# Performance work log

Hardware: AMD Instinct MI355X
Metric: run time of the kernel (lower is better)

Reference implementation:

```python
import jax, jax.numpy as jnp
from jax import lax
import numpy as np

K = 3  # kernel size per dim, dimension=6 -> 3**6 = 729 taps
OFFS = np.stack(np.meshgrid(*([np.arange(K)] * 6), indexing='ij'), axis=-1).reshape(-1, 6).astype(np.int32)


def conv6d(x, kernel):
    """Dense emulation of a 1->1 channel MinkowskiConvolution over 6 spatial dims.

    x: (b, s, s, d, d, d, d) with zeros at absent sparse coordinates.
    kernel: (729,) flattened 3^6 kernel (in=out=1 channel, no bias).
    Zeros at absent coordinates contribute nothing to the gathered sums, so the
    dense conv equals the sparse conv evaluated everywhere.
    """
    xp = jnp.pad(x, [(0, 0)] + [(1, 1)] * 6)
    offs = jnp.asarray(OFFS)
    zero = jnp.int32(0)

    def body(acc, ow):
        off, wt = ow
        sl = lax.dynamic_slice(
            xp, (zero, off[0], off[1], off[2], off[3], off[4], off[5]), x.shape)
        return acc + wt * sl, None

    acc, _ = lax.scan(jax.checkpoint(body), jnp.zeros_like(x), (offs, kernel))
    return acc


def _transpose6d(t):
    # swap the two scale dims and the two image-coordinate pairs:
    # (b, s1, s2, h1, w1, h2, w2) -> (b, s2, s1, h2, w2, h1, w1)
    return jnp.transpose(t, (0, 2, 1, 5, 6, 3, 4))


def setup_inputs() -> dict:
    key = jax.random.key(0)
    k1, k2 = jax.random.split(key)
    x = jax.random.normal(k1, (1, 2, 2, 32, 32, 32, 32), dtype=jnp.float32)
    kernel = jax.random.normal(k2, (K ** 6,), dtype=jnp.float32) * 0.05
    return {"x": x, "kernel": kernel}


def reference(x, kernel):
    # MinkowskiConvolution outputs at the input coordinate set; MinkowskiSigmoid
    # acts on features at those coordinates; to_dense() zero-fills elsewhere.
    # Dense equivalent: mask to the input nonzero set.
    mask = (x != 0).astype(x.dtype)
    branch = lambda z: jax.nn.sigmoid(conv6d(jax.nn.relu(z), kernel))
    # symmetric mode: conv(x) + T(conv(T(x))); T(coords(T(x))) == coords(x)
    y = mask * (branch(x) + _transpose6d(branch(_transpose6d(x))))
    b, s1, s2, d1, d2, d3, d4 = y.shape
    y = y.reshape(b, s1 * s2, d1, d2, d3, d4).sum(axis=1)  # (b, h1, w1, h2, w2)
    return y
```

## Files before the change

### kernel.cpp

```cpp
#include <hip/hip_runtime.h>

typedef _Float16 h2 __attribute__((ext_vector_type(2)));

#define X_SLAB   1048576
#define PAD_S3   34
#define PAD_S2   (34*34)
#define PAD_S1   (34*34*34)
#define PAD_SLAB (34*34*34*34)
#define TAB2_ELEMS (2*81*8)
#define TAB_ELEMS  (4*81*8)

__global__ __launch_bounds__(256)
void prep(const float* __restrict__ x, const float* __restrict__ w,
          h2* __restrict__ rp2, h2* __restrict__ tab2) {
    unsigned gid = blockIdx.x * 256 + threadIdx.x;
    const unsigned total = 2u * PAD_SLAB;
    if (gid < total) {
        unsigned q = gid;
        int j4 = q % 34; q /= 34;
        int j3 = q % 34; q /= 34;
        int j2 = q % 34; q /= 34;
        int j1 = q % 34; q /= 34;
        int tp = q;
        float a = 0.f, b = 0.f;
        if (j1 >= 1 && j1 <= 32 && j2 >= 1 && j2 <= 32 &&
            j3 >= 1 && j3 <= 32 && j4 >= 1 && j4 <= 32) {
            size_t off = (size_t)(j1-1)*32768 + (j2-1)*1024 + (j3-1)*32 + (j4-1);
            a = fmaxf(x[(size_t)(2*tp  )*X_SLAB + off], 0.f);
            b = fmaxf(x[(size_t)(2*tp+1)*X_SLAB + off], 0.f);
        }
        h2 hv; hv.x = (_Float16)a; hv.y = (_Float16)b;
        rp2[gid] = hv;
    }
    if (blockIdx.x == 0) {
        for (int idx = threadIdx.x; idx < TAB2_ELEMS; idx += 256) {
            int n  = idx & 7;
            int r  = idx >> 3;
            int p5 = r % 3; r /= 3;
            int p4 = r % 3; r /= 3;
            int p3 = r % 3; r /= 3;
            int p2 = r % 3; r /= 3;
            int tp = r;
            int br = n & 1, s = n >> 1, s1 = s >> 1, s2 = s & 1;
            float vv[2];
            #pragma unroll
            for (int dt = 0; dt < 2; ++dt) {
                int t = 2*tp + dt, t1 = t >> 1, t2 = t & 1;
                int a2 = t1 - s1 + 1, b2 = t2 - s2 + 1;
                int widx = (br == 0)
                    ? (a2*243 + b2*81 + p2*27 + p3*9 + p4*3 + p5)
                    : (b2*243 + a2*81 + p4*27 + p5*9 + p2*3 + p3);
                vv[dt] = w[widx];
            }
            h2 hw; hw.x = (_Float16)vv[0]; hw.y = (_Float16)vv[1];
            tab2[idx] = hw;
        }
    }
}

__global__ __launch_bounds__(256)
void conv_dot2(const float* __restrict__ x,
               const h2* __restrict__ rp2,
               const h2* __restrict__ tab2,
               float* __restrict__ out) {
    const int e4 = threadIdx.x;
    const int e3 = blockIdx.x * 8 + threadIdx.y;
    const int e2 = blockIdx.y;
    const int e1 = blockIdx.z;

    float acc[8];
    #pragma unroll
    for (int n = 0; n < 8; ++n) acc[n] = 0.f;

    #pragma unroll 1
    for (int tp = 0; tp < 2; ++tp) {
        const h2* st  = rp2 + (size_t)tp * PAD_SLAB;
        const h2* wt0 = tab2 + tp * 648;
        #pragma unroll
        for (int p2 = 0; p2 < 3; ++p2) {
            #pragma unroll
            for (int p3 = 0; p3 < 3; ++p3) {
                const h2* base = st + ((e1+p2)*PAD_S1 + (e2+p3)*PAD_S2
                                       + e3*PAD_S3 + e4);
                const h2* wt = wt0 + (p2*3 + p3) * 72;
                #pragma unroll
                for (int p4 = 0; p4 < 3; ++p4) {
                    #pragma unroll
                    for (int p5 = 0; p5 < 3; ++p5) {
                        h2 v = base[p4*PAD_S3 + p5];
                        const h2* w8 = wt + (p4*3 + p5)*8;
                        #pragma unroll
                        for (int n = 0; n < 8; ++n)
                            acc[n] = __builtin_amdgcn_fdot2(v, w8[n], acc[n], false);
                    }
                }
            }
        }
    }

    const size_t eflat = (size_t)e1*32768 + e2*1024 + e3*32 + e4;
    float res = 0.f;
    #pragma unroll
    for (int i = 0; i < 4; ++i) {
        float xv = x[(size_t)i * X_SLAB + eflat];
        float s0 = __builtin_amdgcn_rcpf(1.f + __expf(-acc[2*i]));
        float s1 = __builtin_amdgcn_rcpf(1.f + __expf(-acc[2*i+1]));
        float m  = (xv != 0.f) ? 1.f : 0.f;
        res = fmaf(m, s0 + s1, res);
    }
    out[eflat] = res;
}

__global__ void build_wtab(const float* __restrict__ w, float* __restrict__ tab) {
    int idx = blockIdx.x * blockDim.x + threadIdx.x;
    if (idx >= TAB_ELEMS) return;
    int n  = idx & 7;
    int r  = idx >> 3;
    int p5 = r % 3; r /= 3;
    int p4 = r % 3; r /= 3;
    int p3 = r % 3; r /= 3;
    int p2 = r % 3; r /= 3;
    int t  = r;
    int t1 = t >> 1, t2 = t & 1;
    int br = n & 1;
    int s  = n >> 1;
    int s1 = s >> 1, s2 = s & 1;
    int a = t1 - s1 + 1;
    int b = t2 - s2 + 1;
    int widx = (br == 0)
        ? (a*243 + b*81 + p2*27 + p3*9 + p4*3 + p5)
        : (b*243 + a*81 + p4*27 + p5*9 + p2*3 + p3);
    tab[idx] = w[widx];
}

__global__ __launch_bounds__(256)
void conv_fp32(const float* __restrict__ x,
               const float* __restrict__ tab,
               float* __restrict__ out) {
    const int e4 = threadIdx.x;
    const int e3 = blockIdx.x * 8 + threadIdx.y;
    const int e2 = blockIdx.y;
    const int e1 = blockIdx.z;

    float acc[8];
    #pragma unroll
    for (int n = 0; n < 8; ++n) acc[n] = 0.f;

    #pragma unroll 1
    for (int t = 0; t < 4; ++t) {
        const float* st  = x + (size_t)t * X_SLAB;
        const float* wt0 = tab + t * 648;
        #pragma unroll
        for (int p2 = 0; p2 < 3; ++p2) {
            #pragma unroll
            for (int p3 = 0; p3 < 3; ++p3) {
                int i1 = e1 + p2 - 1, i2 = e2 + p3 - 1;
                bool v12 = ((unsigned)i1 < 32u) && ((unsigned)i2 < 32u);
                const float* base = st + (i1*32768 + i2*1024 + (e3-1)*32 + (e4-1));
                const float* wt = wt0 + (p2*3 + p3) * 72;
                #pragma unroll
                for (int p4 = 0; p4 < 3; ++p4) {
                    int i3 = e3 + p4 - 1;
                    bool v3 = v12 && ((unsigned)i3 < 32u);
                    #pragma unroll
                    for (int p5 = 0; p5 < 3; ++p5) {
                        int i4 = e4 + p5 - 1;
                        bool ok = v3 && ((unsigned)i4 < 32u);
                        float v = ok ? fmaxf(base[p4*32 + p5], 0.f) : 0.f;
                        const float* w8 = wt + (p4*3 + p5)*8;
                        #pragma unroll
                        for (int n = 0; n < 8; ++n)
                            acc[n] = fmaf(w8[n], v, acc[n]);
                    }
                }
            }
        }
    }

    const size_t eflat = (size_t)e1*32768 + e2*1024 + e3*32 + e4;
    float res = 0.f;
    #pragma unroll
    for (int i = 0; i < 4; ++i) {
        float xv = x[(size_t)i * X_SLAB + eflat];
        float s0 = __builtin_amdgcn_rcpf(1.f + __expf(-acc[2*i]));
        float s1 = __builtin_amdgcn_rcpf(1.f + __expf(-acc[2*i+1]));
        float m  = (xv != 0.f) ? 1.f : 0.f;
        res = fmaf(m, s0 + s1, res);
    }
    out[eflat] = res;
}

extern "C" void kernel_launch(void* const* d_in, const int* in_sizes, int n_in,
                              void* d_out, int out_size, void* d_ws, size_t ws_size,
                              hipStream_t stream) {
    const float* x = (const float*)d_in[0];
    const float* w = (const float*)d_in[1];
    float* out = (float*)d_out;

    const size_t need = 16384 + (size_t)2 * PAD_SLAB * sizeof(h2);
    dim3 blk(32, 8, 1), grd(4, 32, 32);

    if (ws_size >= need) {
        h2* tab2 = (h2*)d_ws;
        h2* rp2  = (h2*)((char*)d_ws + 16384);
        unsigned total = 2u * PAD_SLAB;
        prep<<<dim3((total + 255)/256), dim3(256), 0, stream>>>(x, w, rp2, tab2);
        conv_dot2<<<grd, blk, 0, stream>>>(x, rp2, tab2, out);
    } else {
        float* tab = (float*)d_ws;
        build_wtab<<<dim3((TAB_ELEMS + 255)/256), dim3(256), 0, stream>>>(w, tab);
        conv_fp32<<<grd, blk, 0, stream>>>(x, tab, out);
    }
}
```

Baseline: 114.5 us.

## Register-block four outputs per thread in fp16 dot2 conv with vector row loads

Each thread of the packed-fp16 convolution now computes four consecutive outputs along the innermost dimension. For each kernel row it loads three 8-byte vectors of padded input and reuses them across the three innermost taps, which removes redundant per-tap global loads. The launch shape changes to a 2D grid of 1024 blocks, and the mask load and output store are widened to float4. The cost is more accumulator registers per thread (32 floats) and a quarter as many threads, so occupancy and latency hiding may drop.

```diff
diff --git a/kernel.cpp b/kernel.cpp
--- a/kernel.cpp
+++ b/kernel.cpp
@@ -1,6 +1,8 @@
 #include <hip/hip_runtime.h>
 
 typedef _Float16 h2 __attribute__((ext_vector_type(2)));
+typedef _Float16 h4 __attribute__((ext_vector_type(4)));
+typedef float f4 __attribute__((ext_vector_type(4)));
 
 #define X_SLAB   1048576
 #define PAD_S3   34
@@ -63,52 +65,71 @@
                const h2* __restrict__ rp2,
                const h2* __restrict__ tab2,
                float* __restrict__ out) {
-    const int e4 = threadIdx.x;
-    const int e3 = blockIdx.x * 8 + threadIdx.y;
-    const int e2 = blockIdx.y;
-    const int e1 = blockIdx.z;
-
-    float acc[8];
-    #pragma unroll
-    for (int n = 0; n < 8; ++n) acc[n] = 0.f;
+    const int E4 = threadIdx.x * 4;
+    const int e3 = threadIdx.y;
+    const int e2 = blockIdx.x;
+    const int e1 = blockIdx.y;
+
+    float acc[4][8];
+    #pragma unroll
+    for (int q = 0; q < 4; ++q)
+        #pragma unroll
+        for (int n = 0; n < 8; ++n) acc[q][n] = 0.f;
 
     #pragma unroll 1
     for (int tp = 0; tp < 2; ++tp) {
-        const h2* st  = rp2 + (size_t)tp * PAD_SLAB;
-        const h2* wt0 = tab2 + tp * 648;
-        #pragma unroll
+        #pragma unroll 1
         for (int p2 = 0; p2 < 3; ++p2) {
-            #pragma unroll
+            #pragma unroll 1
             for (int p3 = 0; p3 < 3; ++p3) {
-                const h2* base = st + ((e1+p2)*PAD_S1 + (e2+p3)*PAD_S2
-                                       + e3*PAD_S3 + e4);
-                const h2* wt = wt0 + (p2*3 + p3) * 72;
+                const h2* bp = rp2 + (size_t)tp*PAD_SLAB + (e1+p2)*PAD_S1
+                             + (e2+p3)*PAD_S2 + e3*PAD_S3 + E4;
+                const h2* wt = tab2 + (tp*9 + p2*3 + p3) * 72;
                 #pragma unroll
                 for (int p4 = 0; p4 < 3; ++p4) {
+                    const h4* row = (const h4*)(bp + p4*PAD_S3);
+                    h4 A = row[0];
+                    h4 B = row[1];
+                    h4 C = row[2];
+                    h2 v[6];
+                    v[0] = __builtin_shufflevector(A, A, 0, 1);
+                    v[1] = __builtin_shufflevector(A, A, 2, 3);
+                    v[2] = __builtin_shufflevector(B, B, 0, 1);
+                    v[3] = __builtin_shufflevector(B, B, 2, 3);
+                    v[4] = __builtin_shufflevector(C, C, 0, 1);
+                    v[5] = __builtin_shufflevector(C, C, 2, 3);
                     #pragma unroll
                     for (int p5 = 0; p5 < 3; ++p5) {
-                        h2 v = base[p4*PAD_S3 + p5];
                         const h2* w8 = wt + (p4*3 + p5)*8;
                         #pragma unroll
-                        for (int n = 0; n < 8; ++n)
-                            acc[n] = __builtin_amdgcn_fdot2(v, w8[n], acc[n], false);
+                        for (int q = 0; q < 4; ++q) {
+                            h2 hv = v[q + p5];
+                            #pragma unroll
+                            for (int n = 0; n < 8; ++n)
+                                acc[q][n] = __builtin_amdgcn_fdot2(hv, w8[n],
+                                                                  acc[q][n], false);
+                        }
                     }
                 }
             }
         }
     }
 
-    const size_t eflat = (size_t)e1*32768 + e2*1024 + e3*32 + e4;
-    float res = 0.f;
+    const size_t eflat = (size_t)e1*32768 + e2*1024 + e3*32 + E4;
+    float res[4] = {0.f, 0.f, 0.f, 0.f};
     #pragma unroll
     for (int i = 0; i < 4; ++i) {
-        float xv = x[(size_t)i * X_SLAB + eflat];
-        float s0 = __builtin_amdgcn_rcpf(1.f + __expf(-acc[2*i]));
-        float s1 = __builtin_amdgcn_rcpf(1.f + __expf(-acc[2*i+1]));
-        float m  = (xv != 0.f) ? 1.f : 0.f;
-        res = fmaf(m, s0 + s1, res);
-    }
-    out[eflat] = res;
+        f4 xv = *(const f4*)(x + (size_t)i*X_SLAB + eflat);
+        #pragma unroll
+        for (int q = 0; q < 4; ++q) {
+            float s0 = __builtin_amdgcn_rcpf(1.f + __expf(-acc[q][2*i]));
+            float s1 = __builtin_amdgcn_rcpf(1.f + __expf(-acc[q][2*i+1]));
+            float m  = (xv[q] != 0.f) ? 1.f : 0.f;
+            res[q] = fmaf(m, s0 + s1, res[q]);
+        }
+    }
+    f4 r4; r4.x = res[0]; r4.y = res[1]; r4.z = res[2]; r4.w = res[3];
+    *(f4*)(out + eflat) = r4;
 }
 
 __global__ void build_wtab(const float* __restrict__ w, float* __restrict__ tab) {
@@ -198,17 +219,18 @@
     float* out = (float*)d_out;
 
     const size_t need = 16384 + (size_t)2 * PAD_SLAB * sizeof(h2);
-    dim3 blk(32, 8, 1), grd(4, 32, 32);
 
     if (ws_size >= need) {
         h2* tab2 = (h2*)d_ws;
         h2* rp2  = (h2*)((char*)d_ws + 16384);
         unsigned total = 2u * PAD_SLAB;
         prep<<<dim3((total + 255)/256), dim3(256), 0, stream>>>(x, w, rp2, tab2);
+        dim3 blk(8, 32, 1), grd(32, 32, 1);
         conv_dot2<<<grd, blk, 0, stream>>>(x, rp2, tab2, out);
     } else {
         float* tab = (float*)d_ws;
         build_wtab<<<dim3((TAB_ELEMS + 255)/256), dim3(256), 0, stream>>>(w, tab);
+        dim3 blk(32, 8, 1), grd(4, 32, 32);
         conv_fp32<<<grd, blk, 0, stream>>>(x, tab, out);
     }
 }
```

Measured after the change: 112.3 us. About the same (-1.9%).
